# Kernel optimization log

Hardware: AMD Instinct MI355X
Metric: run time of the kernel (lower is better)

The kernel has to match this reference:

```python
import jax, jax.numpy as jnp
import numpy as np
from jax import lax

TIME_STEPS = 49          # saves at t = 1..49
STEPS_PER_SAVE = 100     # dt = 0.01 -> 100 Euler steps per unit time
DT = 0.01
B = 8192                 # Monte-Carlo batch
EPS = 1e-7


def setup_inputs() -> dict:
    key = jax.random.key(0)
    condition = jax.random.uniform(key, (B, 4), dtype=jnp.float32)
    return {"condition": condition, "seed": 0}


def _simulate(inf, rec, mr, vol, noise):
    # inf/rec/mr/vol: [B]; noise: [TIME_STEPS, STEPS_PER_SAVE, B] ~ N(0, DT)
    r0_mean = inf / rec
    s0 = jnp.full_like(inf, 0.99)
    i0 = jnp.full_like(inf, 0.01)
    r0_ = jnp.zeros_like(inf)
    y0 = (s0, i0, r0_, r0_mean)  # y0[3] = infection_rate / recovery_rate

    def euler_step(carry, dw):  # dw: [B]
        s, i, r, r0 = carry
        newly_infected = r0 * rec * s
        newly_recovered = rec * i
        s_n = s - DT * newly_infected
        i_n = i + DT * (newly_infected - newly_recovered)
        r_n = r + DT * newly_recovered
        # drift mean-reversion + diffusion scaled by sqrt(|r0|)
        r0_n = r0 + DT * mr * (r0_mean - r0) + jnp.sqrt(jnp.abs(r0)) * vol * dw
        return (s_n, i_n, r_n, r0_n), None

    def save_block(carry, dws):  # dws: [STEPS_PER_SAVE, B]
        carry, _ = lax.scan(euler_step, carry, dws)
        return carry, carry[1]  # save infected fraction at integer times

    _, infected = lax.scan(save_block, y0, noise)  # [TIME_STEPS, B]
    return jnp.nan_to_num(infected, nan=0.0, posinf=0.0, neginf=0.0).T  # [B, T]


def _summarize(x, u):
    # x: [B, TIME_STEPS] infected trajectory, u: [B] uniform
    x = jnp.clip(x, 1e-5)
    max_ = x.max(axis=1)
    max_at = (jnp.argmax(x, axis=1).astype(x.dtype) + u) / TIME_STEPS
    vol = jnp.std(jnp.diff(jnp.log(x), axis=1), axis=1)
    s_loc = jnp.array([0.38, 0.21, 0.14], dtype=x.dtype)
    s_scale = jnp.array([0.14, 0.12, 0.03], dtype=x.dtype)
    s = jnp.stack([max_, max_at, vol], axis=-1)  # [B, 3]
    return (s - s_loc) / s_scale


def reference(condition, seed):
    p = jnp.clip(condition, EPS, 1.0 - EPS)  # [B, 4]
    inf, rec, mr, vol = p[:, 0], p[:, 1], p[:, 2], p[:, 3]
    k_noise, k_u = jax.random.split(jax.random.key(seed))
    noise = jax.random.normal(
        k_noise, (TIME_STEPS, STEPS_PER_SAVE, B), dtype=jnp.float32
    ) * jnp.sqrt(jnp.float32(DT))
    infected = _simulate(inf, rec, mr, vol, noise)  # [B, TIME_STEPS]
    u = jax.random.uniform(k_u, (B,), dtype=jnp.float32)
    return _summarize(infected, u)  # [B, 3]
```

## Files before the change

### kernel.cpp

```cpp
#include <hip/hip_runtime.h>
#include <cstdint>

#pragma clang fp contract(off)

#define TSAVES 49
#define SPSAVE 100
#define NB 8192
#define TRAJ 32
#define GENW 14

typedef float f32x4 __attribute__((ext_vector_type(4)));

__device__ __forceinline__ uint32_t rotl32(uint32_t v, int d) {
  return __builtin_rotateleft32(v, (uint32_t)d);
}

__device__ __forceinline__ void tf2x32(uint32_t k0, uint32_t k1,
                                       uint32_t x0, uint32_t x1,
                                       uint32_t& o0, uint32_t& o1) {
  uint32_t ks2 = k0 ^ k1 ^ 0x1BD11BDAu;
#define TF_ROUND(r) { x0 += x1; x1 = rotl32(x1, r); x1 ^= x0; }
  x0 += k0; x1 += k1;
  TF_ROUND(13) TF_ROUND(15) TF_ROUND(26) TF_ROUND(6)
  x0 += k1; x1 += ks2 + 1u;
  TF_ROUND(17) TF_ROUND(29) TF_ROUND(16) TF_ROUND(24)
  x0 += ks2; x1 += k0 + 2u;
  TF_ROUND(13) TF_ROUND(15) TF_ROUND(26) TF_ROUND(6)
  x0 += k0; x1 += k1 + 3u;
  TF_ROUND(17) TF_ROUND(29) TF_ROUND(16) TF_ROUND(24)
  x0 += k1; x1 += ks2 + 4u;
  TF_ROUND(13) TF_ROUND(15) TF_ROUND(26) TF_ROUND(6)
  x0 += ks2; x1 += k0 + 5u;
#undef TF_ROUND
  o0 = x0; o1 = x1;
}

__device__ __forceinline__ void derive_keys(int seed, uint32_t& kn0, uint32_t& kn1,
                                            uint32_t& ku0, uint32_t& ku1) {
  uint64_t sv = (uint64_t)(int64_t)seed;
  uint32_t k0 = (uint32_t)(sv >> 32);
  uint32_t k1 = (uint32_t)(sv & 0xffffffffULL);
  tf2x32(k0, k1, 0u, 0u, kn0, kn1);
  tf2x32(k0, k1, 0u, 1u, ku0, ku1);
}

__device__ __forceinline__ uint32_t rand_bits32(uint32_t k0, uint32_t k1, uint32_t n) {
  uint32_t y0, y1;
  tf2x32(k0, k1, 0u, n, y0, y1);
  return y0 ^ y1;
}

__device__ __forceinline__ float bits_to_eu(uint32_t bits) {
#pragma clang fp contract(fast)
  float u01 = __uint_as_float((bits >> 9) | 0x3f800000u) - 1.0f;
  float u = u01 * 2.0f + (-0.99999994f);
  u = fmaxf(-0.99999994f, u);
  float omu2 = 1.0f - u * u;
  float w = -(__builtin_amdgcn_logf(omu2) * 0.6931472f);
  float p;
  if (w < 5.0f) {
    float z = w - 2.5f;
    p = 2.81022636e-08f;
    p = 3.43273939e-07f + p * z;
    p = -3.5233877e-06f + p * z;
    p = -4.39150654e-06f + p * z;
    p = 0.00021858087f + p * z;
    p = -0.00125372503f + p * z;
    p = -0.00417768164f + p * z;
    p = 0.246640727f + p * z;
    p = 1.50140941f + p * z;
  } else {
    float z = __builtin_amdgcn_sqrtf(w) - 3.0f;
    p = -0.000200214257f;
    p = 0.000100950558f + p * z;
    p = 0.00134934322f + p * z;
    p = -0.00367342844f + p * z;
    p = 0.00573950773f + p * z;
    p = -0.0076224613f + p * z;
    p = 0.00943887047f + p * z;
    p = 1.00167406f + p * z;
    p = 2.83297682f + p * z;
  }
  return p * u;
}

__device__ __forceinline__ float clip_param(float x) {
  return fminf(0.99999988f, fmaxf(1e-07f, x));
}

__global__ __launch_bounds__(1024) void fused_kernel(const float* __restrict__ cond,
                                                     const int* __restrict__ seedp,
                                                     float* __restrict__ out) {
  __shared__ f32x4 nbuf[2][25][TRAJ];
  __shared__ f32x4 rbuf[2][25][TRAJ];
  __shared__ int flags[GENW + 2];

  const int tid = threadIdx.x;
  const int lane = tid & 63;
  const int wv = tid >> 6;
  const int bbase = blockIdx.x * TRAJ;
  const int tr = lane & 31;
  const int h = lane >> 5;
  const int b = bbase + tr;

  if (tid < GENW + 2) flags[tid] = 0;
  __syncthreads();
  volatile int* vflags = flags;

  uint32_t kn0, kn1, ku0, ku1;
  derive_keys(seedp[0], kn0, kn1, ku0, ku1);

  float pinf = clip_param(cond[b * 4 + 0]);
  float prec = clip_param(cond[b * 4 + 1]);
  float pmr  = clip_param(cond[b * 4 + 2]);
  float pvol = clip_param(cond[b * 4 + 3]);
  const float r0m  = pinf / prec;
  const float dtmr = 0.01f * pmr;
  const float c4 = 1.0f - dtmr;
  const float a4 = dtmr * r0m;
  const float c2 = 0.01f * prec;
  const float c3 = 1.0f - c2;
  const float c3p4 = (c3 * c3) * (c3 * c3);
  const float cpv = 0.14142136f * pvol;

  if (wv < GENW) {
    for (int g = 0; g <= 48; ++g) {
      if (g >= 2) {
        while (vflags[GENW] < g - 1) __builtin_amdgcn_s_sleep(1);
      }
      const uint32_t nbase = (uint32_t)(g * SPSAVE) * (uint32_t)NB + (uint32_t)b;
      float* nb = (float*)&nbuf[g & 1][0][0];
#pragma unroll
      for (int k = 0; k < 4; ++k) {
        const int id = wv + GENW * k;
        if (id < 50) {
          const int c = id >> 1;
          const int e = ((id & 1) << 1) | h;
          uint32_t n = nbase + (uint32_t)(4 * c + e) * (uint32_t)NB;
          float eu = bits_to_eu(rand_bits32(kn0, kn1, n));
          nb[(c * 32 + tr) * 4 + e] = eu * cpv;
        }
      }
      __threadfence_block();
      if (lane == 0) vflags[wv] = g + 1;
    }
  } else if (wv == GENW) {
    float r0 = r0m;
    for (int g = 0; g <= 48; ++g) {
      for (;;) {
        int mn = vflags[0];
#pragma unroll
        for (int w = 1; w < GENW; ++w) { int v = vflags[w]; mn = (v < mn) ? v : mn; }
        if (mn >= g + 1) break;
        __builtin_amdgcn_s_sleep(1);
      }
      if (g >= 2) {
        while (vflags[GENW + 1] < g - 1) __builtin_amdgcn_s_sleep(1);
      }
      __threadfence_block();
      const int src = g & 1;
      f32x4 vd = nbuf[src][0][tr];
#pragma unroll
      for (int c = 0; c < 25; ++c) {
        f32x4 vdn = (c < 24) ? nbuf[src][c + 1][tr] : vd;
        f32x4 w;
#pragma unroll
        for (int e = 0; e < 4; ++e) {
          float sq  = __builtin_amdgcn_sqrtf(fabsf(r0));
          float r0h = fmaf(c4, r0, a4);
          r0 = fmaf(sq, vd[e], r0h);
          w[e] = r0;
        }
        rbuf[src][c][tr] = w;
        vd = vdn;
      }
      __threadfence_block();
      if (lane == 0) vflags[GENW] = g + 1;
    }
  } else {
    float s = 0.99f, i = 0.01f, r0in = r0m;
    float best = -1.0f; int bi = 0;
    float plg = 0.0f, sd = 0.0f, sd2 = 0.0f;
    for (int g = 0; g <= 48; ++g) {
      while (vflags[GENW] < g + 1) __builtin_amdgcn_s_sleep(1);
      __threadfence_block();
      const int src = g & 1;
      f32x4 rv = rbuf[src][0][tr];
#pragma unroll
      for (int c = 0; c < 25; ++c) {
        f32x4 rvn = (c < 24) ? rbuf[src][c + 1][tr] : rv;
        float rs0 = r0in * s;  s = fmaf(-c2, rs0, s);
        float rs1 = rv[0] * s; s = fmaf(-c2, rs1, s);
        float rs2 = rv[1] * s; s = fmaf(-c2, rs2, s);
        float rs3 = rv[2] * s; s = fmaf(-c2, rs3, s);
        float hh = fmaf(c3, rs0, rs1);
        hh = fmaf(c3, hh, rs2);
        hh = fmaf(c3, hh, rs3);
        i = fmaf(c3p4, i, c2 * hh);
        r0in = rv[3];
        rv = rvn;
      }
      float v = i;
      if (!isfinite(v)) v = 0.0f;
      float x = fmaxf(v, 1e-05f);
      if (x > best) { best = x; bi = g; }
      float lg = __builtin_amdgcn_logf(x) * 0.6931472f;
      if (g > 0) { float d = lg - plg; sd += d; sd2 += d * d; }
      plg = lg;
      __threadfence_block();
      if (lane == 0) vflags[GENW + 1] = g + 1;
    }
    if (lane < TRAJ) {
      uint32_t ub = rand_bits32(ku0, ku1, (uint32_t)b);
      float u = __uint_as_float((ub >> 9) | 0x3f800000u) - 1.0f;
      u = fmaxf(0.0f, u);
      float maxat = ((float)bi + u) / 49.0f;
      float mean = sd / 48.0f;
      float var = sd2 / 48.0f - mean * mean;
      float stdv = sqrtf(fmaxf(var, 0.0f));
      out[b * 3 + 0] = (best  - 0.38f) / 0.14f;
      out[b * 3 + 1] = (maxat - 0.21f) / 0.12f;
      out[b * 3 + 2] = (stdv  - 0.14f) / 0.03f;
    }
  }
}

extern "C" void kernel_launch(void* const* d_in, const int* in_sizes, int n_in,
                              void* d_out, int out_size, void* d_ws, size_t ws_size,
                              hipStream_t stream) {
  const float* cond = (const float*)d_in[0];
  const int* seedp = (const int*)d_in[1];
  float* out = (float*)d_out;
  (void)d_ws; (void)ws_size;
  fused_kernel<<<NB / TRAJ, 1024, 0, stream>>>(cond, seedp, out);
}
```

Baseline: 150.2 us.

## Quadruple-buffer noise and replace per-wave flags with atomic done counters

Raises the noise buffer from double to quadruple buffering so generator waves can run up to three save blocks ahead of the r0 wave. Replaces the per-generator-wave flag array, which the r0 wave had to scan with a 14-way min, with per-block atomic completion counters polled through a single LDS word. The aim is to cut stalls and polling overhead between the producer and consumer waves, at the cost of more LDS use (another 25.6KB) and atomic traffic.

```diff
diff --git a/kernel.cpp b/kernel.cpp
--- a/kernel.cpp
+++ b/kernel.cpp
@@ -91,9 +91,10 @@
 __global__ __launch_bounds__(1024) void fused_kernel(const float* __restrict__ cond,
                                                      const int* __restrict__ seedp,
                                                      float* __restrict__ out) {
-  __shared__ f32x4 nbuf[2][25][TRAJ];
+  __shared__ f32x4 nbuf[4][25][TRAJ];
   __shared__ f32x4 rbuf[2][25][TRAJ];
-  __shared__ int flags[GENW + 2];
+  __shared__ int done[TSAVES];
+  __shared__ int r0cnt, sicnt;
 
   const int tid = threadIdx.x;
   const int lane = tid & 63;
@@ -103,9 +104,13 @@
   const int h = lane >> 5;
   const int b = bbase + tr;
 
-  if (tid < GENW + 2) flags[tid] = 0;
+  if (tid < TSAVES) done[tid] = 0;
+  if (tid == 0) { r0cnt = 0; sicnt = 0; }
   __syncthreads();
-  volatile int* vflags = flags;
+
+  volatile int* vdone = done;
+  volatile int* vr0 = &r0cnt;
+  volatile int* vsi = &sicnt;
 
   uint32_t kn0, kn1, ku0, ku1;
   derive_keys(seedp[0], kn0, kn1, ku0, ku1);
@@ -125,11 +130,11 @@
 
   if (wv < GENW) {
     for (int g = 0; g <= 48; ++g) {
-      if (g >= 2) {
-        while (vflags[GENW] < g - 1) __builtin_amdgcn_s_sleep(1);
+      if (g >= 4) {
+        while (*vr0 < g - 3) __builtin_amdgcn_s_sleep(1);
       }
       const uint32_t nbase = (uint32_t)(g * SPSAVE) * (uint32_t)NB + (uint32_t)b;
-      float* nb = (float*)&nbuf[g & 1][0][0];
+      float* nb = (float*)&nbuf[g & 3][0][0];
 #pragma unroll
       for (int k = 0; k < 4; ++k) {
         const int id = wv + GENW * k;
@@ -142,27 +147,21 @@
         }
       }
       __threadfence_block();
-      if (lane == 0) vflags[wv] = g + 1;
+      if (lane == 0) atomicAdd(&done[g], 1);
     }
   } else if (wv == GENW) {
     float r0 = r0m;
     for (int g = 0; g <= 48; ++g) {
-      for (;;) {
-        int mn = vflags[0];
-#pragma unroll
-        for (int w = 1; w < GENW; ++w) { int v = vflags[w]; mn = (v < mn) ? v : mn; }
-        if (mn >= g + 1) break;
-        __builtin_amdgcn_s_sleep(1);
-      }
+      while (vdone[g] < GENW) __builtin_amdgcn_s_sleep(1);
       if (g >= 2) {
-        while (vflags[GENW + 1] < g - 1) __builtin_amdgcn_s_sleep(1);
-      }
-      __threadfence_block();
-      const int src = g & 1;
-      f32x4 vd = nbuf[src][0][tr];
+        while (*vsi < g - 1) __builtin_amdgcn_s_sleep(1);
+      }
+      __threadfence_block();
+      const int sn = g & 3, sr = g & 1;
+      f32x4 vd = nbuf[sn][0][tr];
 #pragma unroll
       for (int c = 0; c < 25; ++c) {
-        f32x4 vdn = (c < 24) ? nbuf[src][c + 1][tr] : vd;
+        f32x4 vdn = (c < 24) ? nbuf[sn][c + 1][tr] : vd;
         f32x4 w;
 #pragma unroll
         for (int e = 0; e < 4; ++e) {
@@ -171,24 +170,24 @@
           r0 = fmaf(sq, vd[e], r0h);
           w[e] = r0;
         }
-        rbuf[src][c][tr] = w;
+        rbuf[sr][c][tr] = w;
         vd = vdn;
       }
       __threadfence_block();
-      if (lane == 0) vflags[GENW] = g + 1;
+      if (lane == 0) *vr0 = g + 1;
     }
   } else {
     float s = 0.99f, i = 0.01f, r0in = r0m;
     float best = -1.0f; int bi = 0;
     float plg = 0.0f, sd = 0.0f, sd2 = 0.0f;
     for (int g = 0; g <= 48; ++g) {
-      while (vflags[GENW] < g + 1) __builtin_amdgcn_s_sleep(1);
-      __threadfence_block();
-      const int src = g & 1;
-      f32x4 rv = rbuf[src][0][tr];
+      while (*vr0 < g + 1) __builtin_amdgcn_s_sleep(1);
+      __threadfence_block();
+      const int sr = g & 1;
+      f32x4 rv = rbuf[sr][0][tr];
 #pragma unroll
       for (int c = 0; c < 25; ++c) {
-        f32x4 rvn = (c < 24) ? rbuf[src][c + 1][tr] : rv;
+        f32x4 rvn = (c < 24) ? rbuf[sr][c + 1][tr] : rv;
         float rs0 = r0in * s;  s = fmaf(-c2, rs0, s);
         float rs1 = rv[0] * s; s = fmaf(-c2, rs1, s);
         float rs2 = rv[1] * s; s = fmaf(-c2, rs2, s);
@@ -208,7 +207,7 @@
       if (g > 0) { float d = lg - plg; sd += d; sd2 += d * d; }
       plg = lg;
       __threadfence_block();
-      if (lane == 0) vflags[GENW + 1] = g + 1;
+      if (lane == 0) *vsi = g + 1;
     }
     if (lane < TRAJ) {
       uint32_t ub = rand_bits32(ku0, ku1, (uint32_t)b);
```

Result: faster. 143.0 us (-4.8%).
